# Kernel optimization log

Hardware: AMD Instinct MI355X
Metric: run time of the kernel (lower is better)

Reference implementation:

```python
import jax, jax.numpy as jnp
import numpy as np

# --- GLIF3 / AlphaPSC constants (from NeuronParam / NetworkConfig) ---
N = 2048            # n_neuron
NE = int(N * 0.8)   # excitatory count = 1638
NUM_IN_NEU = 1024
NUM_OUT_NEU = 128
T, B, NUM_IN, NUM_OUT = 100, 64, 784, 10
V_TH, V_RESET = -45.0, -60.0
C_M, TAU = 2.0, 20.0
K_ASC, ASC_AMP = 1.0 / 80.0, -0.2
TAU_REF, BASE_I = 2.0, 0.12
DT = 1.0


def _spike(x):
    # heaviside spike (Erf surrogate only matters for backward)
    return (x >= 0).astype(x.dtype)


def setup_inputs() -> dict:
    key = jax.random.key(0)
    k1, k2, k3, k4 = jax.random.split(key, 4)
    x = jax.random.normal(k1, (T, B, NUM_IN), jnp.float32)
    W_in = jax.random.normal(k2, (NUM_IN_NEU, NUM_IN), jnp.float32) / np.sqrt(NUM_IN)
    W_rec = jax.random.normal(k3, (N, N), jnp.float32) * (5.0 / np.sqrt(N))  # rec_weight_scaling
    W_out = jax.random.normal(k4, (NUM_OUT, NUM_OUT_NEU), jnp.float32) / np.sqrt(NUM_OUT_NEU)
    # replicate NetworkConfig.__post_init__ index sampling (same RandomState, same order)
    rand = np.random.RandomState(32)
    input_indices = jnp.asarray(rand.choice(NE, NUM_IN_NEU, replace=False), jnp.int32)
    output_indices = jnp.asarray(rand.choice(NE, NUM_OUT_NEU, replace=False), jnp.int32)
    tau_syn = jnp.concatenate([jnp.full((NE,), 5.8, jnp.float32),
                               jnp.full((N - NE,), 6.5, jnp.float32)])
    return dict(x=x, W_in=W_in, W_rec=W_rec, W_out=W_out, tau_syn=tau_syn,
                input_indices=input_indices, output_indices=output_indices)


def _run(x, W_in, W_rec, W_out, tau_syn, input_indices, output_indices, spike_fn):
    Tn, Bn, _ = x.shape
    # input projection then scatter into the excitatory input subset
    proj = jnp.einsum('tbi,ni->tbn', x, W_in)                   # (T, B, num_input_neuron)
    inp = jnp.zeros((Tn, Bn, N), x.dtype).at[..., input_indices].set(proj)
    d_syn = jnp.exp(-DT / tau_syn)                              # (N,) per-neuron alpha decay
    e_tau = jnp.e / tau_syn                                     # alpha-kernel peak normalization
    d_asc = jnp.exp(-K_ASC * DT)

    def step(carry, inp_t):
        v, psc, rise, asc, ref, spk = carry
        # recurrent connection + external drive feeds the alpha synapse
        I_in = spk @ W_rec.T + inp_t                            # (B, N)
        psc_n = d_syn * (psc + DT * rise)                       # alpha-PSC (dual-exp) update
        rise_n = d_syn * rise + e_tau * I_in
        asc_n = d_asc * asc + ASC_AMP * spk                     # after-spike current
        active = (ref <= 0).astype(v.dtype)                     # refractory gate
        dv = (psc_n + asc_n + BASE_I) / C_M - (v - V_RESET) / TAU
        v_n = v + active * DT * dv
        spk_n = spike_fn(v_n - V_TH) * active
        v_n = v_n - spk_n * (V_TH - V_RESET)                    # soft reset (hard_reset=False)
        ref_n = jnp.where(spk_n > 0, TAU_REF, jnp.maximum(ref - DT, 0.0))
        return (v_n, psc_n, rise_n, asc_n, ref_n, spk_n), spk_n

    z = jnp.zeros((Bn, N), x.dtype)
    c0 = (jnp.full((Bn, N), V_RESET, x.dtype), z, z, z, z, z)
    _, spikes = jax.lax.scan(step, c0, inp)                     # spikes: (T, B, N)
    rate = spikes[..., output_indices].mean(axis=0)             # (B, num_output_neuron)
    return rate @ W_out.T                                       # (B, num_output)


def reference(x, W_in, W_rec, W_out, tau_syn, input_indices, output_indices):
    return _run(x, W_in, W_rec, W_out, tau_syn, input_indices, output_indices, _spike)
```

## Files before the change

kernel.cpp:

```cpp
#include <hip/hip_runtime.h>
#include <math.h>

#define N_NEU    2048
#define BB       64
#define TT       100
#define KIN      784
#define NIN_NEU  1024
#define N_OUT    10
#define NOUT_NEU 128

typedef unsigned int u32;
typedef unsigned long long u64;
typedef unsigned short u16;
typedef double f64x4 __attribute__((ext_vector_type(4)));

__global__ void k_prep(const float* __restrict__ tau, double* __restrict__ d_syn,
                       double* __restrict__ e_tau, int* __restrict__ inv){
    int n = blockIdx.x * blockDim.x + threadIdx.x;
    if(n < N_NEU){
        double tv = (double)tau[n];
        d_syn[n] = exp(-1.0 / tv);
        e_tau[n] = 2.718281828459045 / tv;
        inv[n] = -1;
    }
}

__global__ void k_scatter(const int* __restrict__ idx, int* __restrict__ inv){
    int j = blockIdx.x * blockDim.x + threadIdx.x;
    if(j < NIN_NEU) inv[idx[j]] = j;
}

__global__ void k_zero(u64* __restrict__ exch, int nexch){
    int j = blockIdx.x * blockDim.x + threadIdx.x;
    if(j < nexch) exch[j] = 0ull;
}

__global__ void k_probe(int* __restrict__ flag){
    int l = threadIdx.x & 63;
    double a = (double)((l & 15)*4 + (l >> 4) + 1);
    double b = (double)((l >> 4)*16 + (l & 15) + 1);
    f64x4 acc = {0.0, 0.0, 0.0, 0.0};
    acc = __builtin_amdgcn_mfma_f64_16x16x4f64(a, b, acc, 0, 0, 0);
    bool oka = true, okb = true;
    int j = l & 15;
    #pragma unroll
    for(int r=0;r<4;r++){
        int ia = 4*(l >> 4) + r;
        int ib = (l >> 4) + 4*r;
        double expA = 0.0, expB = 0.0;
        #pragma unroll
        for(int k=0;k<4;k++){
            expA += (double)((4*ia + k + 1) * (16*k + j + 1));
            expB += (double)((4*ib + k + 1) * (16*k + j + 1));
        }
        oka = oka && (acc[r] == expA);
        okb = okb && (acc[r] == expB);
    }
    bool alla = __all(oka), allb = __all(okb);
    if(threadIdx.x == 0) *flag = alla ? 0 : (allb ? 1 : 2);
}

__global__ __launch_bounds__(256) void k_tr(const float* __restrict__ Wrec, float* __restrict__ Wt){
    __shared__ float tile[32][33];
    int bx = blockIdx.x, by = blockIdx.y;
    int txx = threadIdx.x, tyy = threadIdx.y;
    #pragma unroll
    for(int j=0;j<4;j++)
        tile[tyy+8*j][txx] = Wrec[(size_t)(by*32 + tyy+8*j)*N_NEU + bx*32 + txx];
    __syncthreads();
    #pragma unroll
    for(int j=0;j<4;j++)
        Wt[(size_t)(bx*32 + tyy+8*j)*N_NEU + by*32 + txx] = tile[txx][tyy+8*j];
}

__global__ __launch_bounds__(256) void k_proj_mfma(const float* __restrict__ X, const float* __restrict__ Win,
                                                   const int* __restrict__ flagp, double* __restrict__ projC){
    const int flag = *flagp;
    if(flag >= 2) return;
    __shared__ float As[32][81];
    __shared__ float Bs[32][81];
    const int t   = blockIdx.x;
    const int c0  = blockIdx.y * 64;
    const int tid = threadIdx.x;
    const int w   = tid >> 6;
    const int l   = tid & 63;
    const int g   = l >> 4;
    const int cl  = l & 15;
    const int lr  = tid >> 2;
    const int lk  = (tid & 3) * 8;

    f64x4 acc[4] = {{0.,0.,0.,0.},{0.,0.,0.,0.},{0.,0.,0.,0.},{0.,0.,0.,0.}};

    for(int k0 = 0; k0 < KIN; k0 += 32){
        int kk = k0 + lk;
        float a8[8], b8[8];
        if(kk + 8 <= KIN){
            const float* pa = X   + (size_t)(t*64 + lr)*KIN + kk;
            const float* pb = Win + (size_t)(c0 + lr)*KIN + kk;
            float4 ra0 = *reinterpret_cast<const float4*>(pa);
            float4 ra1 = *reinterpret_cast<const float4*>(pa + 4);
            float4 rb0 = *reinterpret_cast<const float4*>(pb);
            float4 rb1 = *reinterpret_cast<const float4*>(pb + 4);
            a8[0]=ra0.x; a8[1]=ra0.y; a8[2]=ra0.z; a8[3]=ra0.w;
            a8[4]=ra1.x; a8[5]=ra1.y; a8[6]=ra1.z; a8[7]=ra1.w;
            b8[0]=rb0.x; b8[1]=rb0.y; b8[2]=rb0.z; b8[3]=rb0.w;
            b8[4]=rb1.x; b8[5]=rb1.y; b8[6]=rb1.z; b8[7]=rb1.w;
        } else {
            #pragma unroll
            for(int e=0;e<8;e++){ a8[e]=0.0f; b8[e]=0.0f; }
        }
        #pragma unroll
        for(int e=0;e<8;e++){ As[lk+e][lr] = a8[e]; Bs[lk+e][lr] = b8[e]; }
        __syncthreads();

        #pragma unroll
        for(int kq=0;kq<8;kq++){
            double a = (double)As[kq*4 + g][w*16 + cl];
            #pragma unroll
            for(int ct=0;ct<4;ct++){
                double bb = (double)Bs[kq*4 + g][ct*16 + cl];
                acc[ct] = __builtin_amdgcn_mfma_f64_16x16x4f64(a, bb, acc[ct], 0, 0, 0);
            }
        }
        __syncthreads();
    }

    #pragma unroll
    for(int ct=0;ct<4;ct++){
        int c = c0 + ct*16 + cl;
        #pragma unroll
        for(int j=0;j<4;j++){
            int b = w*16 + ((flag == 0) ? (4*g + j) : (g + 4*j));
            projC[((size_t)b*TT + t)*NIN_NEU + c] = acc[ct][j];
        }
    }
}

__global__ __launch_bounds__(256) void k_proj_valu(const float* __restrict__ X, const float* __restrict__ Win,
                                                   const int* __restrict__ flagp, double* __restrict__ projC){
    if(*flagp < 2) return;
    __shared__ float As[32][68];
    __shared__ float Bs[32][68];
    const int r0 = blockIdx.x * 64;
    const int c0 = blockIdx.y * 64;
    const int t  = threadIdx.x;
    const int lr = t >> 2;
    const int lk = (t & 3) * 8;
    const int tx = t & 15, ty = t >> 4;
    double acc[4][4] = {};
    for(int k0 = 0; k0 < KIN; k0 += 32){
        int kk = k0 + lk;
        float a8[8], b8[8];
        if(kk + 8 <= KIN){
            const float* pa = X   + (size_t)(r0+lr)*KIN + kk;
            const float* pb = Win + (size_t)(c0+lr)*KIN + kk;
            float4 ra0 = *reinterpret_cast<const float4*>(pa);
            float4 ra1 = *reinterpret_cast<const float4*>(pa + 4);
            float4 rb0 = *reinterpret_cast<const float4*>(pb);
            float4 rb1 = *reinterpret_cast<const float4*>(pb + 4);
            a8[0]=ra0.x; a8[1]=ra0.y; a8[2]=ra0.z; a8[3]=ra0.w;
            a8[4]=ra1.x; a8[5]=ra1.y; a8[6]=ra1.z; a8[7]=ra1.w;
            b8[0]=rb0.x; b8[1]=rb0.y; b8[2]=rb0.z; b8[3]=rb0.w;
            b8[4]=rb1.x; b8[5]=rb1.y; b8[6]=rb1.z; b8[7]=rb1.w;
        } else {
            #pragma unroll
            for(int e=0;e<8;e++){ a8[e]=0.0f; b8[e]=0.0f; }
        }
        #pragma unroll
        for(int e=0;e<8;e++){ As[lk+e][lr] = a8[e]; Bs[lk+e][lr] = b8[e]; }
        __syncthreads();
        #pragma unroll
        for(int kkk=0;kkk<32;kkk++){
            float4 af = *reinterpret_cast<const float4*>(&As[kkk][ty*4]);
            float4 bf = *reinterpret_cast<const float4*>(&Bs[kkk][tx*4]);
            double a[4] = {(double)af.x,(double)af.y,(double)af.z,(double)af.w};
            double b[4] = {(double)bf.x,(double)bf.y,(double)bf.z,(double)bf.w};
            #pragma unroll
            for(int i=0;i<4;i++)
                #pragma unroll
                for(int j=0;j<4;j++)
                    acc[i][j] += a[i]*b[j];
        }
        __syncthreads();
    }
    const int tt = blockIdx.x;
    #pragma unroll
    for(int j=0;j<4;j++){
        int c = c0 + tx*4 + j;
        #pragma unroll
        for(int i=0;i<4;i++){
            int b = ty*4 + i;
            projC[((size_t)b*TT + tt)*NIN_NEU + c] = acc[i][j];
        }
    }
}

__global__ __launch_bounds__(512) void k_sim(
        const double* __restrict__ projC, const float* __restrict__ Wt,
        const double* __restrict__ dsyn, const double* __restrict__ etau,
        const int* __restrict__ inv,
        u64* __restrict__ exch, double* __restrict__ cntout){
    __shared__ double Ip[4][512];
    __shared__ u32 words[64];
    __shared__ u16 list[N_NEU];
    __shared__ int cntS;

    const int bid = blockIdx.x;
    const int b   = bid >> 2;
    const int q   = bid & 3;
    const int tid = threadIdx.x;
    const int n   = q*512 + tid;
    const int team = tid >> 7;
    const int c4   = (tid & 127) * 4;
    const float*  WtQ   = Wt + q*512;
    const double* projB = projC + (size_t)b*TT*NIN_NEU;

    u64* myE = exch + (size_t)bid*32;

    const double ds = dsyn[n], et = etau[n];
    const int jv = inv[n];
    const double dasc = exp(-0.0125);
    double v=-60.0, psc=0.0, rise=0.0, asc=0.0, ref=0.0, spk=0.0, creg=0.0;

    if(tid == 0) cntS = 0;
    __syncthreads();

    for(int t=0;t<TT;t++){
        double pp = (jv >= 0) ? projB[(size_t)t*NIN_NEU + jv] : 0.0;

        const int cc  = cntS;
        const int beg = (cc * team)     >> 2;
        const int end = (cc * (team+1)) >> 2;
        double I[4] = {0.0, 0.0, 0.0, 0.0};
        int i = beg;
        for(; i + 8 <= end; i += 8){
            int m[8];
            #pragma unroll
            for(int u=0;u<8;u++) m[u] = list[i+u];
            float4 wv[8];
            #pragma unroll
            for(int u=0;u<8;u++)
                wv[u] = *reinterpret_cast<const float4*>(WtQ + ((size_t)m[u] << 11) + c4);
            #pragma unroll
            for(int u=0;u<8;u++){
                I[0] += (double)wv[u].x; I[1] += (double)wv[u].y;
                I[2] += (double)wv[u].z; I[3] += (double)wv[u].w;
            }
        }
        for(; i < end; ++i){
            int mm = list[i];
            float4 w4 = *reinterpret_cast<const float4*>(WtQ + ((size_t)mm << 11) + c4);
            I[0] += (double)w4.x; I[1] += (double)w4.y;
            I[2] += (double)w4.z; I[3] += (double)w4.w;
        }
        #pragma unroll
        for(int u=0;u<4;u++) Ip[team][c4+u] = I[u];
        __syncthreads();

        double Irec = Ip[0][tid] + Ip[1][tid] + Ip[2][tid] + Ip[3][tid] + pp;

        double psc_n  = ds * (psc + rise);
        double rise_n = ds * rise + et * Irec;
        double asc_n  = dasc * asc + (-0.2) * spk;
        double act    = (ref <= 0.0) ? 1.0 : 0.0;
        double dv  = (psc_n + asc_n + 0.12) / 2.0 - (v - (-60.0)) / 20.0;
        double v_n = v + act * dv;
        double s_n = ((v_n - (-45.0)) >= 0.0) ? act : 0.0;
        v_n = v_n - s_n * 15.0;
        double ref_n = (s_n > 0.0) ? 2.0 : fmax(ref - 1.0, 0.0);
        v = v_n; psc = psc_n; rise = rise_n; asc = asc_n; ref = ref_n; spk = s_n;
        creg += s_n;

        u64 bal = __ballot(s_n > 0.0);
        int w = tid >> 6, lane = tid & 63;
        u64 tagv = ((u64)(t+1)) << 32;
        if(lane == 0){
            u32 lo = (u32)bal, hi = (u32)(bal >> 32);
            words[q*16 + 2*w]     = lo;
            words[q*16 + 2*w + 1] = hi;
            u64* dst = myE + (size_t)(t & 1)*16;
            atomicExch(&dst[2*w],     tagv | (u64)lo);
            atomicExch(&dst[2*w + 1], tagv | (u64)hi);
        }
        if(tid < 48){
            int pidx = tid >> 4;
            int w2   = tid & 15;
            int q2   = pidx + (pidx >= q ? 1 : 0);
            u64* src = exch + (size_t)(b*4 + q2)*32 + (size_t)(t & 1)*16;
            u64 val = atomicAdd(&src[w2], 0ull);
            while((val >> 32) != (u64)(t+1)){
                __builtin_amdgcn_s_sleep(1);
                val = atomicAdd(&src[w2], 0ull);
            }
            words[q2*16 + w2] = (u32)val;
        }
        __syncthreads();

        if(tid < 64){
            u32 wv = words[tid];
            int c = __popc(wv);
            int incl = c;
            #pragma unroll
            for(int off=1; off<64; off<<=1){
                int x = __shfl_up(incl, off);
                if(tid >= off) incl += x;
            }
            int excl = incl - c;
            u32 z = wv;
            int base = tid * 32;
            while(z){
                int bp = __ffs(z) - 1;
                z &= z - 1;
                list[excl++] = (u16)(base + bp);
            }
            if(tid == 63) cntS = incl;
        }
        __syncthreads();
    }

    cntout[(size_t)b*N_NEU + n] = creg;
}

__global__ void k_final(const double* __restrict__ cnt, const int* __restrict__ oidx,
                        const float* __restrict__ Wout, float* __restrict__ out){
    int i = blockIdx.x * blockDim.x + threadIdx.x;
    if(i >= BB * N_OUT) return;
    int b = i / N_OUT, o = i - b * N_OUT;
    double accv = 0.0;
    for(int j=0;j<NOUT_NEU;j++){
        double rate = cnt[(size_t)b*N_NEU + oidx[j]] / 100.0;
        accv += rate * (double)Wout[o*NOUT_NEU + j];
    }
    out[i] = (float)accv;
}

extern "C" void kernel_launch(void* const* d_in, const int* in_sizes, int n_in,
                              void* d_out, int out_size, void* d_ws, size_t ws_size,
                              hipStream_t stream){
    const float* X    = (const float*)d_in[0];
    const float* Win  = (const float*)d_in[1];
    const float* Wrec = (const float*)d_in[2];
    const float* Wout = (const float*)d_in[3];
    const float* tau  = (const float*)d_in[4];
    const int*   iidx = (const int*)d_in[5];
    const int*   oidx = (const int*)d_in[6];
    float* out = (float*)d_out;

    char* w = (char*)d_ws;
    const size_t OFF_PROJ = 0;
    const size_t OFF_CNT  = OFF_PROJ + (size_t)BB*TT*NIN_NEU*8;
    const size_t OFF_WT   = OFF_CNT + (size_t)BB*N_NEU*8;
    const size_t OFF_EXCH = OFF_WT + (size_t)N_NEU*N_NEU*4;
    const size_t OFF_DS   = OFF_EXCH + 65536;
    const size_t OFF_ET   = OFF_DS + N_NEU*8;
    const size_t OFF_INV  = OFF_ET + N_NEU*8;
    const size_t OFF_FLAG = OFF_INV + N_NEU*4;

    double* projC = (double*)(w + OFF_PROJ);
    double* cnt   = (double*)(w + OFF_CNT);
    float*  Wt    = (float*)(w + OFF_WT);
    u64*    exch  = (u64*)(w + OFF_EXCH);
    double* dsyn  = (double*)(w + OFF_DS);
    double* etau  = (double*)(w + OFF_ET);
    int*    inv   = (int*)(w + OFF_INV);
    int*    flag  = (int*)(w + OFF_FLAG);

    k_prep     <<<dim3(8),      dim3(256),  0, stream>>>(tau, dsyn, etau, inv);
    k_scatter  <<<dim3(4),      dim3(256),  0, stream>>>(iidx, inv);
    k_zero     <<<dim3(32),     dim3(256),  0, stream>>>(exch, 8192);
    k_probe    <<<dim3(1),      dim3(64),   0, stream>>>(flag);
    k_tr       <<<dim3(64,64),  dim3(32,8), 0, stream>>>(Wrec, Wt);
    k_proj_mfma<<<dim3(100,16), dim3(256),  0, stream>>>(X, Win, flag, projC);
    k_proj_valu<<<dim3(100,16), dim3(256),  0, stream>>>(X, Win, flag, projC);
    k_sim      <<<dim3(4*BB),   dim3(512),  0, stream>>>(projC, Wt, dsyn, etau, inv, exch, cnt);
    k_final    <<<dim3(3),      dim3(256),  0, stream>>>(cnt, oidx, Wout, out);
}
```

Measured before the change: 573.5 us.

## Fuse projection and simulation into one kernel with per-timestep readiness counters

Merges the input projection GEMM and the recurrent spiking simulation into one launch. Projection blocks publish each timestep's results through atomic exchanges and bump a per-timestep counter, and simulation blocks spin on that counter before consuming the step, so the scan can start before the whole projection finishes. Projection blocks are reshaped to 512 threads with smaller per-warp tiles, and the separate MFMA and VALU projection launches are removed. The risks are deadlock if simulation blocks fill the GPU before the projection blocks are scheduled (this relies on block dispatch order), plus extra atomic load traffic on the projection reads inside the sim loop.

```diff
diff --git a/kernel.cpp b/kernel.cpp
--- a/kernel.cpp
+++ b/kernel.cpp
@@ -8,6 +8,8 @@
 #define NIN_NEU  1024
 #define N_OUT    10
 #define NOUT_NEU 128
+#define SIMBLK   256
+#define PROJBLK  1600
 
 typedef unsigned int u32;
 typedef unsigned long long u64;
@@ -30,9 +32,10 @@
     if(j < NIN_NEU) inv[idx[j]] = j;
 }
 
-__global__ void k_zero(u64* __restrict__ exch, int nexch){
+__global__ void k_zero(u64* __restrict__ exch, int nexch, u32* __restrict__ pcnt, int ncnt){
     int j = blockIdx.x * blockDim.x + threadIdx.x;
     if(j < nexch) exch[j] = 0ull;
+    if(j < ncnt)  pcnt[j] = 0u;
 }
 
 __global__ void k_probe(int* __restrict__ flag){
@@ -73,252 +76,233 @@
         Wt[(size_t)(bx*32 + tyy+8*j)*N_NEU + by*32 + txx] = tile[txx][tyy+8*j];
 }
 
-__global__ __launch_bounds__(256) void k_proj_mfma(const float* __restrict__ X, const float* __restrict__ Win,
-                                                   const int* __restrict__ flagp, double* __restrict__ projC){
-    const int flag = *flagp;
-    if(flag >= 2) return;
-    __shared__ float As[32][81];
-    __shared__ float Bs[32][81];
-    const int t   = blockIdx.x;
-    const int c0  = blockIdx.y * 64;
-    const int tid = threadIdx.x;
-    const int w   = tid >> 6;
-    const int l   = tid & 63;
-    const int g   = l >> 4;
-    const int cl  = l & 15;
-    const int lr  = tid >> 2;
-    const int lk  = (tid & 3) * 8;
-
-    f64x4 acc[4] = {{0.,0.,0.,0.},{0.,0.,0.,0.},{0.,0.,0.,0.},{0.,0.,0.,0.}};
-
-    for(int k0 = 0; k0 < KIN; k0 += 32){
-        int kk = k0 + lk;
-        float a8[8], b8[8];
-        if(kk + 8 <= KIN){
-            const float* pa = X   + (size_t)(t*64 + lr)*KIN + kk;
-            const float* pb = Win + (size_t)(c0 + lr)*KIN + kk;
-            float4 ra0 = *reinterpret_cast<const float4*>(pa);
-            float4 ra1 = *reinterpret_cast<const float4*>(pa + 4);
-            float4 rb0 = *reinterpret_cast<const float4*>(pb);
-            float4 rb1 = *reinterpret_cast<const float4*>(pb + 4);
-            a8[0]=ra0.x; a8[1]=ra0.y; a8[2]=ra0.z; a8[3]=ra0.w;
-            a8[4]=ra1.x; a8[5]=ra1.y; a8[6]=ra1.z; a8[7]=ra1.w;
-            b8[0]=rb0.x; b8[1]=rb0.y; b8[2]=rb0.z; b8[3]=rb0.w;
-            b8[4]=rb1.x; b8[5]=rb1.y; b8[6]=rb1.z; b8[7]=rb1.w;
-        } else {
-            #pragma unroll
-            for(int e=0;e<8;e++){ a8[e]=0.0f; b8[e]=0.0f; }
-        }
-        #pragma unroll
-        for(int e=0;e<8;e++){ As[lk+e][lr] = a8[e]; Bs[lk+e][lr] = b8[e]; }
-        __syncthreads();
-
-        #pragma unroll
-        for(int kq=0;kq<8;kq++){
-            double a = (double)As[kq*4 + g][w*16 + cl];
-            #pragma unroll
-            for(int ct=0;ct<4;ct++){
-                double bb = (double)Bs[kq*4 + g][ct*16 + cl];
-                acc[ct] = __builtin_amdgcn_mfma_f64_16x16x4f64(a, bb, acc[ct], 0, 0, 0);
-            }
-        }
-        __syncthreads();
-    }
-
-    #pragma unroll
-    for(int ct=0;ct<4;ct++){
-        int c = c0 + ct*16 + cl;
-        #pragma unroll
-        for(int j=0;j<4;j++){
-            int b = w*16 + ((flag == 0) ? (4*g + j) : (g + 4*j));
-            projC[((size_t)b*TT + t)*NIN_NEU + c] = acc[ct][j];
-        }
-    }
-}
-
-__global__ __launch_bounds__(256) void k_proj_valu(const float* __restrict__ X, const float* __restrict__ Win,
-                                                   const int* __restrict__ flagp, double* __restrict__ projC){
-    if(*flagp < 2) return;
-    __shared__ float As[32][68];
-    __shared__ float Bs[32][68];
-    const int r0 = blockIdx.x * 64;
-    const int c0 = blockIdx.y * 64;
-    const int t  = threadIdx.x;
-    const int lr = t >> 2;
-    const int lk = (t & 3) * 8;
-    const int tx = t & 15, ty = t >> 4;
-    double acc[4][4] = {};
-    for(int k0 = 0; k0 < KIN; k0 += 32){
-        int kk = k0 + lk;
-        float a8[8], b8[8];
-        if(kk + 8 <= KIN){
-            const float* pa = X   + (size_t)(r0+lr)*KIN + kk;
-            const float* pb = Win + (size_t)(c0+lr)*KIN + kk;
-            float4 ra0 = *reinterpret_cast<const float4*>(pa);
-            float4 ra1 = *reinterpret_cast<const float4*>(pa + 4);
-            float4 rb0 = *reinterpret_cast<const float4*>(pb);
-            float4 rb1 = *reinterpret_cast<const float4*>(pb + 4);
-            a8[0]=ra0.x; a8[1]=ra0.y; a8[2]=ra0.z; a8[3]=ra0.w;
-            a8[4]=ra1.x; a8[5]=ra1.y; a8[6]=ra1.z; a8[7]=ra1.w;
-            b8[0]=rb0.x; b8[1]=rb0.y; b8[2]=rb0.z; b8[3]=rb0.w;
-            b8[4]=rb1.x; b8[5]=rb1.y; b8[6]=rb1.z; b8[7]=rb1.w;
-        } else {
-            #pragma unroll
-            for(int e=0;e<8;e++){ a8[e]=0.0f; b8[e]=0.0f; }
-        }
-        #pragma unroll
-        for(int e=0;e<8;e++){ As[lk+e][lr] = a8[e]; Bs[lk+e][lr] = b8[e]; }
-        __syncthreads();
-        #pragma unroll
-        for(int kkk=0;kkk<32;kkk++){
-            float4 af = *reinterpret_cast<const float4*>(&As[kkk][ty*4]);
-            float4 bf = *reinterpret_cast<const float4*>(&Bs[kkk][tx*4]);
-            double a[4] = {(double)af.x,(double)af.y,(double)af.z,(double)af.w};
-            double b[4] = {(double)bf.x,(double)bf.y,(double)bf.z,(double)bf.w};
-            #pragma unroll
-            for(int i=0;i<4;i++)
-                #pragma unroll
-                for(int j=0;j<4;j++)
-                    acc[i][j] += a[i]*b[j];
-        }
-        __syncthreads();
-    }
-    const int tt = blockIdx.x;
-    #pragma unroll
-    for(int j=0;j<4;j++){
-        int c = c0 + tx*4 + j;
-        #pragma unroll
-        for(int i=0;i<4;i++){
-            int b = ty*4 + i;
-            projC[((size_t)b*TT + tt)*NIN_NEU + c] = acc[i][j];
-        }
-    }
-}
-
-__global__ __launch_bounds__(512) void k_sim(
-        const double* __restrict__ projC, const float* __restrict__ Wt,
+__global__ __launch_bounds__(512, 4) void k_mega(
+        const float* __restrict__ X, const float* __restrict__ Win,
+        const int* __restrict__ flagp,
+        double* __restrict__ projC, const float* __restrict__ Wt,
         const double* __restrict__ dsyn, const double* __restrict__ etau,
         const int* __restrict__ inv,
-        u64* __restrict__ exch, double* __restrict__ cntout){
-    __shared__ double Ip[4][512];
-    __shared__ u32 words[64];
-    __shared__ u16 list[N_NEU];
-    __shared__ int cntS;
-
-    const int bid = blockIdx.x;
-    const int b   = bid >> 2;
-    const int q   = bid & 3;
+        u64* __restrict__ exch, u32* __restrict__ projCnt,
+        double* __restrict__ cntout){
+    __shared__ __align__(16) char smem[20992];
+
+    if(blockIdx.x >= PROJBLK){
+        double (*Ip)[512] = (double(*)[512])smem;
+        u32* words = (u32*)(smem + 16384);
+        u16* list  = (u16*)(smem + 16640);
+        int* cntSp = (int*)(smem + 20736);
+
+        const int bid = blockIdx.x - PROJBLK;
+        const int b   = bid >> 2;
+        const int q   = bid & 3;
+        const int tid = threadIdx.x;
+        const int n   = q*512 + tid;
+        const int team = tid >> 7;
+        const int c4   = (tid & 127) * 4;
+        const float*  WtQ   = Wt + q*512;
+        const double* projB = projC + (size_t)b*TT*NIN_NEU;
+
+        u64* myE = exch + (size_t)bid*32;
+
+        const double ds = dsyn[n], et = etau[n];
+        const int jv = inv[n];
+        const double dasc = exp(-0.0125);
+        double v=-60.0, psc=0.0, rise=0.0, asc=0.0, ref=0.0, spk=0.0, creg=0.0;
+
+        if(tid == 0){
+            *cntSp = 0;
+            while(atomicAdd(&projCnt[0], 0u) < 16u) __builtin_amdgcn_s_sleep(2);
+        }
+        __syncthreads();
+
+        for(int t=0;t<TT;t++){
+            double pp = 0.0;
+            if(jv >= 0) pp = atomicAdd((double*)(projB + (size_t)t*NIN_NEU + jv), 0.0);
+
+            const int cc  = *cntSp;
+            const int beg = (cc * team)     >> 2;
+            const int end = (cc * (team+1)) >> 2;
+            double I[4] = {0.0, 0.0, 0.0, 0.0};
+            int i = beg;
+            for(; i + 8 <= end; i += 8){
+                int m[8];
+                #pragma unroll
+                for(int u=0;u<8;u++) m[u] = list[i+u];
+                float4 wv[8];
+                #pragma unroll
+                for(int u=0;u<8;u++)
+                    wv[u] = *reinterpret_cast<const float4*>(WtQ + ((size_t)m[u] << 11) + c4);
+                #pragma unroll
+                for(int u=0;u<8;u++){
+                    I[0] += (double)wv[u].x; I[1] += (double)wv[u].y;
+                    I[2] += (double)wv[u].z; I[3] += (double)wv[u].w;
+                }
+            }
+            for(; i < end; ++i){
+                int mm = list[i];
+                float4 w4 = *reinterpret_cast<const float4*>(WtQ + ((size_t)mm << 11) + c4);
+                I[0] += (double)w4.x; I[1] += (double)w4.y;
+                I[2] += (double)w4.z; I[3] += (double)w4.w;
+            }
+            #pragma unroll
+            for(int u=0;u<4;u++) Ip[team][c4+u] = I[u];
+            __syncthreads();
+
+            double Irec = Ip[0][tid] + Ip[1][tid] + Ip[2][tid] + Ip[3][tid] + pp;
+
+            double psc_n  = ds * (psc + rise);
+            double rise_n = ds * rise + et * Irec;
+            double asc_n  = dasc * asc + (-0.2) * spk;
+            double act    = (ref <= 0.0) ? 1.0 : 0.0;
+            double dv  = (psc_n + asc_n + 0.12) / 2.0 - (v - (-60.0)) / 20.0;
+            double v_n = v + act * dv;
+            double s_n = ((v_n - (-45.0)) >= 0.0) ? act : 0.0;
+            v_n = v_n - s_n * 15.0;
+            double ref_n = (s_n > 0.0) ? 2.0 : fmax(ref - 1.0, 0.0);
+            v = v_n; psc = psc_n; rise = rise_n; asc = asc_n; ref = ref_n; spk = s_n;
+            creg += s_n;
+
+            u64 bal = __ballot(s_n > 0.0);
+            int w = tid >> 6, lane = tid & 63;
+            u64 tagv = ((u64)(t+1)) << 32;
+            if(lane == 0){
+                u32 lo = (u32)bal, hi = (u32)(bal >> 32);
+                words[q*16 + 2*w]     = lo;
+                words[q*16 + 2*w + 1] = hi;
+                u64* dst = myE + (size_t)(t & 1)*16;
+                atomicExch(&dst[2*w],     tagv | (u64)lo);
+                atomicExch(&dst[2*w + 1], tagv | (u64)hi);
+            }
+            if(tid < 48){
+                int pidx = tid >> 4;
+                int w2   = tid & 15;
+                int q2   = pidx + (pidx >= q ? 1 : 0);
+                u64* src = exch + (size_t)(b*4 + q2)*32 + (size_t)(t & 1)*16;
+                u64 val = atomicAdd(&src[w2], 0ull);
+                while((val >> 32) != (u64)(t+1)){
+                    __builtin_amdgcn_s_sleep(1);
+                    val = atomicAdd(&src[w2], 0ull);
+                }
+                words[q2*16 + w2] = (u32)val;
+            } else if(tid == 48 && t+1 < TT){
+                while(atomicAdd(&projCnt[t+1], 0u) < 16u) __builtin_amdgcn_s_sleep(1);
+            }
+            __syncthreads();
+
+            if(tid < 64){
+                u32 wv = words[tid];
+                int c = __popc(wv);
+                int incl = c;
+                #pragma unroll
+                for(int off=1; off<64; off<<=1){
+                    int x = __shfl_up(incl, off);
+                    if(tid >= off) incl += x;
+                }
+                int excl = incl - c;
+                u32 z = wv;
+                int base = tid * 32;
+                while(z){
+                    int bp = __ffs(z) - 1;
+                    z &= z - 1;
+                    list[excl++] = (u16)(base + bp);
+                }
+                if(tid == 63) *cntSp = incl;
+            }
+            __syncthreads();
+        }
+
+        cntout[(size_t)b*N_NEU + n] = creg;
+        return;
+    }
+
+    float (*As)[81] = (float(*)[81])smem;
+    float (*Bs)[81] = (float(*)[81])(smem + 10368);
+    const int bi  = blockIdx.x;
+    const int t   = bi >> 4;
+    const int c0  = (bi & 15) * 64;
     const int tid = threadIdx.x;
-    const int n   = q*512 + tid;
-    const int team = tid >> 7;
-    const int c4   = (tid & 127) * 4;
-    const float*  WtQ   = Wt + q*512;
-    const double* projB = projC + (size_t)b*TT*NIN_NEU;
-
-    u64* myE = exch + (size_t)bid*32;
-
-    const double ds = dsyn[n], et = etau[n];
-    const int jv = inv[n];
-    const double dasc = exp(-0.0125);
-    double v=-60.0, psc=0.0, rise=0.0, asc=0.0, ref=0.0, spk=0.0, creg=0.0;
-
-    if(tid == 0) cntS = 0;
+    const int flag = *flagp;
+    const int lr = tid >> 3;
+    const int lk = (tid & 7) * 4;
+
+    if(flag < 2){
+        const int w   = tid >> 6;
+        const int l   = tid & 63;
+        const int g   = l >> 4;
+        const int cl  = l & 15;
+        const int r0w = (w & 3) * 16;
+        const int cb  = (w >> 2) * 2;
+
+        f64x4 acc[2] = {{0.,0.,0.,0.},{0.,0.,0.,0.}};
+        for(int k0 = 0; k0 < KIN; k0 += 32){
+            int kk = k0 + lk;
+            float a4[4] = {0.f,0.f,0.f,0.f}, b4[4] = {0.f,0.f,0.f,0.f};
+            if(kk + 4 <= KIN){
+                float4 ra = *reinterpret_cast<const float4*>(X   + (size_t)(t*64 + lr)*KIN + kk);
+                float4 rb = *reinterpret_cast<const float4*>(Win + (size_t)(c0 + lr)*KIN + kk);
+                a4[0]=ra.x; a4[1]=ra.y; a4[2]=ra.z; a4[3]=ra.w;
+                b4[0]=rb.x; b4[1]=rb.y; b4[2]=rb.z; b4[3]=rb.w;
+            }
+            #pragma unroll
+            for(int e=0;e<4;e++){ As[lk+e][lr] = a4[e]; Bs[lk+e][lr] = b4[e]; }
+            __syncthreads();
+            #pragma unroll
+            for(int kq=0;kq<8;kq++){
+                double a  = (double)As[kq*4 + g][r0w + cl];
+                double b0 = (double)Bs[kq*4 + g][(cb+0)*16 + cl];
+                double b1 = (double)Bs[kq*4 + g][(cb+1)*16 + cl];
+                acc[0] = __builtin_amdgcn_mfma_f64_16x16x4f64(a, b0, acc[0], 0, 0, 0);
+                acc[1] = __builtin_amdgcn_mfma_f64_16x16x4f64(a, b1, acc[1], 0, 0, 0);
+            }
+            __syncthreads();
+        }
+        #pragma unroll
+        for(int ccq=0;ccq<2;ccq++){
+            int c = c0 + (cb+ccq)*16 + cl;
+            #pragma unroll
+            for(int j=0;j<4;j++){
+                int br = r0w + ((flag == 0) ? (4*g + j) : (g + 4*j));
+                atomicExch((u64*)&projC[((size_t)br*TT + t)*NIN_NEU + c],
+                           __double_as_longlong(acc[ccq][j]));
+            }
+        }
+    } else {
+        const int r2 = (tid >> 4) * 2;
+        const int cf = (tid & 15) * 4;
+        double acc[2][4] = {};
+        for(int k0 = 0; k0 < KIN; k0 += 32){
+            int kk = k0 + lk;
+            float a4[4] = {0.f,0.f,0.f,0.f}, b4[4] = {0.f,0.f,0.f,0.f};
+            if(kk + 4 <= KIN){
+                float4 ra = *reinterpret_cast<const float4*>(X   + (size_t)(t*64 + lr)*KIN + kk);
+                float4 rb = *reinterpret_cast<const float4*>(Win + (size_t)(c0 + lr)*KIN + kk);
+                a4[0]=ra.x; a4[1]=ra.y; a4[2]=ra.z; a4[3]=ra.w;
+                b4[0]=rb.x; b4[1]=rb.y; b4[2]=rb.z; b4[3]=rb.w;
+            }
+            #pragma unroll
+            for(int e=0;e<4;e++){ As[lk+e][lr] = a4[e]; Bs[lk+e][lr] = b4[e]; }
+            __syncthreads();
+            #pragma unroll
+            for(int kkk=0;kkk<32;kkk++){
+                double a0 = (double)As[kkk][r2], a1 = (double)As[kkk][r2+1];
+                #pragma unroll
+                for(int j=0;j<4;j++){
+                    double bb = (double)Bs[kkk][cf+j];
+                    acc[0][j] += a0*bb;
+                    acc[1][j] += a1*bb;
+                }
+            }
+            __syncthreads();
+        }
+        #pragma unroll
+        for(int i2=0;i2<2;i2++)
+            #pragma unroll
+            for(int j=0;j<4;j++)
+                atomicExch((u64*)&projC[((size_t)(r2+i2)*TT + t)*NIN_NEU + c0 + cf + j],
+                           __double_as_longlong(acc[i2][j]));
+    }
     __syncthreads();
-
-    for(int t=0;t<TT;t++){
-        double pp = (jv >= 0) ? projB[(size_t)t*NIN_NEU + jv] : 0.0;
-
-        const int cc  = cntS;
-        const int beg = (cc * team)     >> 2;
-        const int end = (cc * (team+1)) >> 2;
-        double I[4] = {0.0, 0.0, 0.0, 0.0};
-        int i = beg;
-        for(; i + 8 <= end; i += 8){
-            int m[8];
-            #pragma unroll
-            for(int u=0;u<8;u++) m[u] = list[i+u];
-            float4 wv[8];
-            #pragma unroll
-            for(int u=0;u<8;u++)
-                wv[u] = *reinterpret_cast<const float4*>(WtQ + ((size_t)m[u] << 11) + c4);
-            #pragma unroll
-            for(int u=0;u<8;u++){
-                I[0] += (double)wv[u].x; I[1] += (double)wv[u].y;
-                I[2] += (double)wv[u].z; I[3] += (double)wv[u].w;
-            }
-        }
-        for(; i < end; ++i){
-            int mm = list[i];
-            float4 w4 = *reinterpret_cast<const float4*>(WtQ + ((size_t)mm << 11) + c4);
-            I[0] += (double)w4.x; I[1] += (double)w4.y;
-            I[2] += (double)w4.z; I[3] += (double)w4.w;
-        }
-        #pragma unroll
-        for(int u=0;u<4;u++) Ip[team][c4+u] = I[u];
-        __syncthreads();
-
-        double Irec = Ip[0][tid] + Ip[1][tid] + Ip[2][tid] + Ip[3][tid] + pp;
-
-        double psc_n  = ds * (psc + rise);
-        double rise_n = ds * rise + et * Irec;
-        double asc_n  = dasc * asc + (-0.2) * spk;
-        double act    = (ref <= 0.0) ? 1.0 : 0.0;
-        double dv  = (psc_n + asc_n + 0.12) / 2.0 - (v - (-60.0)) / 20.0;
-        double v_n = v + act * dv;
-        double s_n = ((v_n - (-45.0)) >= 0.0) ? act : 0.0;
-        v_n = v_n - s_n * 15.0;
-        double ref_n = (s_n > 0.0) ? 2.0 : fmax(ref - 1.0, 0.0);
-        v = v_n; psc = psc_n; rise = rise_n; asc = asc_n; ref = ref_n; spk = s_n;
-        creg += s_n;
-
-        u64 bal = __ballot(s_n > 0.0);
-        int w = tid >> 6, lane = tid & 63;
-        u64 tagv = ((u64)(t+1)) << 32;
-        if(lane == 0){
-            u32 lo = (u32)bal, hi = (u32)(bal >> 32);
-            words[q*16 + 2*w]     = lo;
-            words[q*16 + 2*w + 1] = hi;
-            u64* dst = myE + (size_t)(t & 1)*16;
-            atomicExch(&dst[2*w],     tagv | (u64)lo);
-            atomicExch(&dst[2*w + 1], tagv | (u64)hi);
-        }
-        if(tid < 48){
-            int pidx = tid >> 4;
-            int w2   = tid & 15;
-            int q2   = pidx + (pidx >= q ? 1 : 0);
-            u64* src = exch + (size_t)(b*4 + q2)*32 + (size_t)(t & 1)*16;
-            u64 val = atomicAdd(&src[w2], 0ull);
-            while((val >> 32) != (u64)(t+1)){
-                __builtin_amdgcn_s_sleep(1);
-                val = atomicAdd(&src[w2], 0ull);
-            }
-            words[q2*16 + w2] = (u32)val;
-        }
-        __syncthreads();
-
-        if(tid < 64){
-            u32 wv = words[tid];
-            int c = __popc(wv);
-            int incl = c;
-            #pragma unroll
-            for(int off=1; off<64; off<<=1){
-                int x = __shfl_up(incl, off);
-                if(tid >= off) incl += x;
-            }
-            int excl = incl - c;
-            u32 z = wv;
-            int base = tid * 32;
-            while(z){
-                int bp = __ffs(z) - 1;
-                z &= z - 1;
-                list[excl++] = (u16)(base + bp);
-            }
-            if(tid == 63) cntS = incl;
-        }
-        __syncthreads();
-    }
-
-    cntout[(size_t)b*N_NEU + n] = creg;
+    if(tid == 0) atomicAdd(&projCnt[t], 1u);
 }
 
 __global__ void k_final(const double* __restrict__ cnt, const int* __restrict__ oidx,
@@ -351,7 +335,8 @@
     const size_t OFF_CNT  = OFF_PROJ + (size_t)BB*TT*NIN_NEU*8;
     const size_t OFF_WT   = OFF_CNT + (size_t)BB*N_NEU*8;
     const size_t OFF_EXCH = OFF_WT + (size_t)N_NEU*N_NEU*4;
-    const size_t OFF_DS   = OFF_EXCH + 65536;
+    const size_t OFF_PCNT = OFF_EXCH + 65536;
+    const size_t OFF_DS   = OFF_PCNT + 512;
     const size_t OFF_ET   = OFF_DS + N_NEU*8;
     const size_t OFF_INV  = OFF_ET + N_NEU*8;
     const size_t OFF_FLAG = OFF_INV + N_NEU*4;
@@ -360,18 +345,18 @@
     double* cnt   = (double*)(w + OFF_CNT);
     float*  Wt    = (float*)(w + OFF_WT);
     u64*    exch  = (u64*)(w + OFF_EXCH);
+    u32*    pcnt  = (u32*)(w + OFF_PCNT);
     double* dsyn  = (double*)(w + OFF_DS);
     double* etau  = (double*)(w + OFF_ET);
     int*    inv   = (int*)(w + OFF_INV);
     int*    flag  = (int*)(w + OFF_FLAG);
 
-    k_prep     <<<dim3(8),      dim3(256),  0, stream>>>(tau, dsyn, etau, inv);
-    k_scatter  <<<dim3(4),      dim3(256),  0, stream>>>(iidx, inv);
-    k_zero     <<<dim3(32),     dim3(256),  0, stream>>>(exch, 8192);
-    k_probe    <<<dim3(1),      dim3(64),   0, stream>>>(flag);
-    k_tr       <<<dim3(64,64),  dim3(32,8), 0, stream>>>(Wrec, Wt);
-    k_proj_mfma<<<dim3(100,16), dim3(256),  0, stream>>>(X, Win, flag, projC);
-    k_proj_valu<<<dim3(100,16), dim3(256),  0, stream>>>(X, Win, flag, projC);
-    k_sim      <<<dim3(4*BB),   dim3(512),  0, stream>>>(projC, Wt, dsyn, etau, inv, exch, cnt);
-    k_final    <<<dim3(3),      dim3(256),  0, stream>>>(cnt, oidx, Wout, out);
-}
+    k_prep   <<<dim3(8),      dim3(256),  0, stream>>>(tau, dsyn, etau, inv);
+    k_scatter<<<dim3(4),      dim3(256),  0, stream>>>(iidx, inv);
+    k_zero   <<<dim3(32),     dim3(256),  0, stream>>>(exch, 8192, pcnt, 128);
+    k_probe  <<<dim3(1),      dim3(64),   0, stream>>>(flag);
+    k_tr     <<<dim3(64,64),  dim3(32,8), 0, stream>>>(Wrec, Wt);
+    k_mega   <<<dim3(PROJBLK + SIMBLK), dim3(512), 0, stream>>>(
+                 X, Win, flag, projC, Wt, dsyn, etau, inv, exch, pcnt, cnt);
+    k_final  <<<dim3(3),      dim3(256),  0, stream>>>(cnt, oidx, Wout, out);
+}
```

Result: slower. 743.9 us (+29.7%).
